# Optimization experiments

Hardware: AMD Instinct MI355X
Metric: run time of the kernel (lower is better)

The kernel has to match this reference:

```python
import jax, jax.numpy as jnp
import numpy as np

B, S, E, H, L = 4, 512, 768, 12, 12
D = E // H
FF = 4 * E
EPS = 1e-5
SCALE = jnp.float32(768.0 ** 0.5)  # emb_size ** (1/2), applied AFTER softmax per source


def setup_inputs() -> dict:
    key = jax.random.key(0)
    ks = jax.random.split(key, 18)
    std = 0.02
    n = lambda k, shp: (jax.random.normal(k, shp, jnp.float32) * std)
    return {
        "x": jax.random.normal(ks[0], (B, S, E), jnp.float32),
        "Wqkv": n(ks[1], (L, E, 3 * E)),
        "bqkv": n(ks[2], (L, 3 * E)),
        "Wp": n(ks[3], (L, E, E)),
        "bp": n(ks[4], (L, E)),
        "W1": n(ks[5], (L, E, FF)),
        "b1": n(ks[6], (L, FF)),
        "W2": n(ks[7], (L, FF, E)),
        "b2": n(ks[8], (L, E)),
        "ln1_g": jnp.ones((L, E), jnp.float32), "ln1_b": jnp.zeros((L, E), jnp.float32),
        "ln2_g": jnp.ones((L, E), jnp.float32), "ln2_b": jnp.zeros((L, E), jnp.float32),
        "ln3_g": jnp.ones((L, E), jnp.float32), "ln3_b": jnp.zeros((L, E), jnp.float32),
        "ln4_g": jnp.ones((L, E), jnp.float32), "ln4_b": jnp.zeros((L, E), jnp.float32),
    }


def _ln(x, g, b):
    m = jnp.mean(x, axis=-1, keepdims=True)
    v = jnp.mean(jnp.square(x - m), axis=-1, keepdims=True)
    return (x - m) * jax.lax.rsqrt(v + EPS) * g + b


def _block(x, p):
    Wqkv, bqkv, Wp, bp, W1, b1, W2, b2, g1, be1, g2, be2, g3, be3, g4, be4 = p
    # --- attention branch ---
    h = _ln(x, g1, be1)
    qkv = h @ Wqkv + bqkv                      # [B,S,3E]
    qkv = qkv.reshape(B, S, H, D, 3)           # qkv is innermost factor in source rearrange
    q = jnp.transpose(qkv[..., 0], (0, 2, 1, 3))  # [B,H,S,D]
    k = jnp.transpose(qkv[..., 1], (0, 2, 1, 3))
    v = jnp.transpose(qkv[..., 2], (0, 2, 1, 3))
    energy = jnp.einsum('bhqd,bhkd->bhqk', q, k)
    att = jax.nn.softmax(energy, axis=-1) / SCALE  # NOTE: scaling AFTER softmax (faithful)
    o = jnp.einsum('bhqk,bhkd->bhqd', att, v)
    o = jnp.transpose(o, (0, 2, 1, 3)).reshape(B, S, E)
    o = o @ Wp + bp
    r1 = _ln(o, g2, be2) + x                   # first ResidualAdd (final LN inside branch)
    # --- feed-forward branch ---
    f = _ln(r1, g3, be3)
    f = jax.nn.gelu(f @ W1 + b1, approximate=False)
    f = f @ W2 + b2
    r2 = _ln(f, g4, be4) + r1                  # second ResidualAdd
    return x + r2                              # outer residual: x = x + block(x)


def reference(x, Wqkv, bqkv, Wp, bp, W1, b1, W2, b2,
              ln1_g, ln1_b, ln2_g, ln2_b, ln3_g, ln3_b, ln4_g, ln4_b):
    params = (Wqkv, bqkv, Wp, bp, W1, b1, W2, b2,
              ln1_g, ln1_b, ln2_g, ln2_b, ln3_g, ln3_b, ln4_g, ln4_b)
    out, _ = jax.lax.scan(lambda c, p: (_block(c, p), None), x, params)
    return out
```

## Files before the change

### kernel.cpp

```cpp
#include <hip/hip_runtime.h>
#include <hip/hip_bf16.h>
#include <stdint.h>

#define LAYERS 12
#define M_ROWS 2048
#define E_DIM 768
#define FF_DIM 3072
#define QKV_DIM 2304
#define SCALE_INV 0.036084391824351615f

typedef __hip_bfloat16 bf16;
typedef __attribute__((ext_vector_type(8))) __bf16 bf16x8;
typedef __attribute__((ext_vector_type(4))) float f32x4;

__device__ __forceinline__ float bf2f(bf16 v) { return __bfloat162float(v); }
__device__ __forceinline__ bf16 f2bf(float v) { return __float2bfloat16(v); }

__device__ __forceinline__ float gelu_f(float x) {
  return 0.5f * x * (1.0f + erff(x * 0.70710678118654752f));
}

__device__ __forceinline__ void glds16(const bf16* g, bf16* l) {
  __builtin_amdgcn_global_load_lds(
      (const __attribute__((address_space(1))) void*)g,
      (__attribute__((address_space(3))) void*)l, 16, 0, 0);
}

__global__ __launch_bounds__(256) void transpose_k(
    const float* __restrict__ w0, const float* __restrict__ w1,
    const float* __restrict__ w2, const float* __restrict__ w3,
    bf16* __restrict__ t0, bf16* __restrict__ t1,
    bf16* __restrict__ t2, bf16* __restrict__ t3)
{
  __shared__ float T[32][33];
  int l = blockIdx.x / 6912;
  int bid = blockIdx.x - l * 6912;
  const float* src; bf16* dst; int K, N, tile;
  if (bid < 1728)      { src = w0 + (size_t)l * 768 * 2304; dst = t0 + (size_t)l * 768 * 2304; K = 768;  N = 2304; tile = bid; }
  else if (bid < 2304) { src = w1 + (size_t)l * 768 * 768;  dst = t1 + (size_t)l * 768 * 768;  K = 768;  N = 768;  tile = bid - 1728; }
  else if (bid < 4608) { src = w2 + (size_t)l * 768 * 3072; dst = t2 + (size_t)l * 768 * 3072; K = 768;  N = 3072; tile = bid - 2304; }
  else                 { src = w3 + (size_t)l * 3072 * 768; dst = t3 + (size_t)l * 3072 * 768; K = 3072; N = 768;  tile = bid - 4608; }
  int tilesN = N >> 5;
  int tk = tile / tilesN;
  int tn = tile - tk * tilesN;
  int tx = threadIdx.x & 31, ty = threadIdx.x >> 5;
  int k0 = tk << 5, n0 = tn << 5;
#pragma unroll
  for (int i = 0; i < 4; i++)
    T[ty + i * 8][tx] = src[(size_t)(k0 + ty + i * 8) * N + n0 + tx];
  __syncthreads();
#pragma unroll
  for (int i = 0; i < 4; i++)
    dst[(size_t)(n0 + ty + i * 8) * K + k0 + tx] = f2bf(T[tx][ty + i * 8]);
}

__device__ __forceinline__ void rowstats(float s, float sq, float* red, int tid,
                                         float& mean, float& rstd) {
#pragma unroll
  for (int off = 32; off; off >>= 1) {
    s += __shfl_xor(s, off);
    sq += __shfl_xor(sq, off);
  }
  __syncthreads();
  int wv = tid >> 6;
  if ((tid & 63) == 0) { red[wv] = s; red[4 + wv] = sq; }
  __syncthreads();
  s  = red[0] + red[1] + red[2] + red[3];
  sq = red[4] + red[5] + red[6] + red[7];
  mean = s * (1.0f / 768.0f);
  float var = sq * (1.0f / 768.0f) - mean * mean;
  rstd = rsqrtf(var + 1e-5f);
}

__global__ __launch_bounds__(256) void ln_k(
    const float* in, const float* gamma, const float* beta, bf16* outp)
{
  __shared__ float red[8];
  int row = blockIdx.x, tid = threadIdx.x;
  const float* x = in + (size_t)row * 768;
  float v[3]; float s = 0.f, sq = 0.f;
#pragma unroll
  for (int j = 0; j < 3; j++) {
    v[j] = x[tid + j * 256];
    s += v[j]; sq += v[j] * v[j];
  }
  float mean, rstd;
  rowstats(s, sq, red, tid, mean, rstd);
#pragma unroll
  for (int j = 0; j < 3; j++) {
    int c = tid + j * 256;
    outp[(size_t)row * 768 + c] = f2bf((v[j] - mean) * rstd * gamma[c] + beta[c]);
  }
}

__global__ __launch_bounds__(256) void ln23_k(
    const float* in, const float* g2, const float* b2, const float* xres,
    float* r1out, const float* g3, const float* b3, bf16* hbout)
{
  __shared__ float red[8];
  int row = blockIdx.x, tid = threadIdx.x;
  const float* x = in + (size_t)row * 768;
  float v[3]; float s = 0.f, sq = 0.f;
#pragma unroll
  for (int j = 0; j < 3; j++) {
    v[j] = x[tid + j * 256];
    s += v[j]; sq += v[j] * v[j];
  }
  float mean, rstd;
  rowstats(s, sq, red, tid, mean, rstd);
  s = 0.f; sq = 0.f;
#pragma unroll
  for (int j = 0; j < 3; j++) {
    int c = tid + j * 256;
    v[j] = (v[j] - mean) * rstd * g2[c] + b2[c] + xres[(size_t)row * 768 + c];
    r1out[(size_t)row * 768 + c] = v[j];
    s += v[j]; sq += v[j] * v[j];
  }
  rowstats(s, sq, red, tid, mean, rstd);
#pragma unroll
  for (int j = 0; j < 3; j++) {
    int c = tid + j * 256;
    hbout[(size_t)row * 768 + c] = f2bf((v[j] - mean) * rstd * g3[c] + b3[c]);
  }
}

__global__ __launch_bounds__(256) void ln41_k(
    const float* in, const float* g4, const float* b4, const float* r1,
    float* xio, const float* g1n, const float* b1n, bf16* hbout)
{
  __shared__ float red[8];
  int row = blockIdx.x, tid = threadIdx.x;
  const float* x = in + (size_t)row * 768;
  float v[3]; float s = 0.f, sq = 0.f;
#pragma unroll
  for (int j = 0; j < 3; j++) {
    v[j] = x[tid + j * 256];
    s += v[j]; sq += v[j] * v[j];
  }
  float mean, rstd;
  rowstats(s, sq, red, tid, mean, rstd);
  s = 0.f; sq = 0.f;
#pragma unroll
  for (int j = 0; j < 3; j++) {
    int c = tid + j * 256;
    size_t idx = (size_t)row * 768 + c;
    v[j] = (v[j] - mean) * rstd * g4[c] + b4[c] + r1[idx] + xio[idx];
    xio[idx] = v[j];
    s += v[j]; sq += v[j] * v[j];
  }
  if (g1n == nullptr) return;
  rowstats(s, sq, red, tid, mean, rstd);
#pragma unroll
  for (int j = 0; j < 3; j++) {
    int c = tid + j * 256;
    hbout[(size_t)row * 768 + c] = f2bf((v[j] - mean) * rstd * g1n[c] + b1n[c]);
  }
}

template<int OUT_MODE>
__global__ __launch_bounds__(256) void gemm128_k(
    const bf16* __restrict__ A, const bf16* __restrict__ BT,
    const float* __restrict__ bias, void* __restrict__ Cout,
    bf16* __restrict__ qo, bf16* __restrict__ ko, bf16* __restrict__ vo,
    int N, int K, int nTilesN)
{
  __shared__ __align__(16) bf16 Als[128 * 32];
  __shared__ __align__(16) bf16 Bls[128 * 32];
  int tid = threadIdx.x;
  int lane = tid & 63, w = tid >> 6;
  int l15 = lane & 15, l4 = lane >> 4;
  int tm = blockIdx.x / nTilesN;
  int tn = blockIdx.x - tm * nTilesN;
  int m0 = tm << 7, n0 = tn << 7;
  int wm = (w >> 1) << 6, wn = (w & 1) << 6;
  const bf16* Ag = A + (size_t)m0 * K;
  const bf16* Bg = BT + (size_t)n0 * K;
  int srow = tid >> 2;
  int scol = (tid & 3) * 8;
  f32x4 acc[4][4] = {};
  for (int k0 = 0; k0 < K; k0 += 32) {
    __syncthreads();
    glds16(Ag + (size_t)srow * K + k0 + scol,        Als + tid * 8);
    glds16(Ag + (size_t)(srow + 64) * K + k0 + scol, Als + 2048 + tid * 8);
    glds16(Bg + (size_t)srow * K + k0 + scol,        Bls + tid * 8);
    glds16(Bg + (size_t)(srow + 64) * K + k0 + scol, Bls + 2048 + tid * 8);
    __syncthreads();
    int ko8 = l4 * 8;
    bf16x8 af[4], bfr[4];
#pragma unroll
    for (int i = 0; i < 4; i++)
      af[i] = *(const bf16x8*)&Als[(wm + i * 16 + l15) * 32 + ko8];
#pragma unroll
    for (int j = 0; j < 4; j++)
      bfr[j] = *(const bf16x8*)&Bls[(wn + j * 16 + l15) * 32 + ko8];
#pragma unroll
    for (int i = 0; i < 4; i++)
#pragma unroll
      for (int j = 0; j < 4; j++)
        acc[i][j] = __builtin_amdgcn_mfma_f32_16x16x32_bf16(af[i], bfr[j], acc[i][j], 0, 0, 0);
  }
#pragma unroll
  for (int i = 0; i < 4; i++) {
    int mbase = m0 + wm + i * 16 + (l4 << 2);
#pragma unroll
    for (int j = 0; j < 4; j++) {
      int n = n0 + wn + j * 16 + l15;
      float bvs = bias[n];
      if (OUT_MODE == 3) {
        int h = n / 192;
        int rm = n - h * 192;
        int d = rm / 3;
        int t = rm - d * 3;
#pragma unroll
        for (int rg = 0; rg < 4; rg++) {
          int m = mbase + rg;
          float val = acc[i][j][rg] + bvs;
          int b = m >> 9, sIdx = m & 511;
          int bh = b * 12 + h;
          if (t == 2)
            vo[(size_t)((bh << 6) + d) * 512 + sIdx] = f2bf(val);
          else {
            bf16* dsts = (t == 0) ? qo : ko;
            dsts[(size_t)((bh << 9) + sIdx) * 64 + d] = f2bf(val);
          }
        }
      } else {
#pragma unroll
        for (int rg = 0; rg < 4; rg++) {
          int m = mbase + rg;
          float val = acc[i][j][rg] + bvs;
          ((bf16*)Cout)[(size_t)m * N + n] = f2bf(gelu_f(val));
        }
      }
    }
  }
}

__global__ __launch_bounds__(256) void gemm64_k(
    const bf16* __restrict__ A, const bf16* __restrict__ BT,
    const float* __restrict__ bias, float* __restrict__ Cout,
    int N, int K, int nTilesN)
{
  __shared__ __align__(16) bf16 Als[64 * 32];
  __shared__ __align__(16) bf16 Bls[64 * 32];
  int tid = threadIdx.x;
  int lane = tid & 63, w = tid >> 6;
  int l15 = lane & 15, l4 = lane >> 4;
  int tm = blockIdx.x / nTilesN;
  int tn = blockIdx.x - tm * nTilesN;
  int m0 = tm << 6, n0 = tn << 6;
  int wm = (w >> 1) << 5, wn = (w & 1) << 5;
  const bf16* Ag = A + (size_t)m0 * K;
  const bf16* Bg = BT + (size_t)n0 * K;
  int srow = tid >> 2;
  int scol = (tid & 3) * 8;
  f32x4 acc[2][2] = {};
  for (int k0 = 0; k0 < K; k0 += 32) {
    __syncthreads();
    glds16(Ag + (size_t)srow * K + k0 + scol, Als + tid * 8);
    glds16(Bg + (size_t)srow * K + k0 + scol, Bls + tid * 8);
    __syncthreads();
    int ko8 = l4 * 8;
    bf16x8 af[2], bfr[2];
#pragma unroll
    for (int i = 0; i < 2; i++)
      af[i] = *(const bf16x8*)&Als[(wm + i * 16 + l15) * 32 + ko8];
#pragma unroll
    for (int j = 0; j < 2; j++)
      bfr[j] = *(const bf16x8*)&Bls[(wn + j * 16 + l15) * 32 + ko8];
#pragma unroll
    for (int i = 0; i < 2; i++)
#pragma unroll
      for (int j = 0; j < 2; j++)
        acc[i][j] = __builtin_amdgcn_mfma_f32_16x16x32_bf16(af[i], bfr[j], acc[i][j], 0, 0, 0);
  }
#pragma unroll
  for (int i = 0; i < 2; i++) {
    int mbase = m0 + wm + i * 16 + (l4 << 2);
#pragma unroll
    for (int j = 0; j < 2; j++) {
      int n = n0 + wn + j * 16 + l15;
      float bvs = bias[n];
#pragma unroll
      for (int rg = 0; rg < 4; rg++)
        Cout[(size_t)(mbase + rg) * N + n] = acc[i][j][rg] + bvs;
    }
  }
}

#define PSTR 80
__global__ __launch_bounds__(256) void attn_k(
    const bf16* __restrict__ q, const bf16* __restrict__ k,
    const bf16* __restrict__ vT, bf16* __restrict__ o)
{
  __shared__ __align__(16) bf16 Kls[64 * 64];
  __shared__ __align__(16) bf16 Vls[64 * 64];
  __shared__ __align__(16) bf16 Pls[4][16 * PSTR];
  int tid = threadIdx.x;
  int lane = tid & 63, w = tid >> 6;
  int l15 = lane & 15, l4 = lane >> 4;
  int qt = blockIdx.x & 7;
  int bh = blockIdx.x >> 3;
  size_t base = (size_t)bh * 32768;

  const bf16* qrowp = q + base + (size_t)(qt * 64 + w * 16 + l15) * 64 + l4 * 8;
  bf16x8 qf0 = *(const bf16x8*)qrowp;
  bf16x8 qf1 = *(const bf16x8*)(qrowp + 32);

  float mrow[4] = {-1e30f, -1e30f, -1e30f, -1e30f};
  float lsum[4] = {0.f, 0.f, 0.f, 0.f};
  f32x4 Oacc[4] = {};
  const f32x4 zed = {0.f, 0.f, 0.f, 0.f};
  bf16* pw = &Pls[w][0];

  for (int kt = 0; kt < 8; kt++) {
    __syncthreads();
#pragma unroll
    for (int rep = 0; rep < 2; rep++) {
      int c = tid + rep * 256;
      int row = c >> 3, col8 = (c & 7) * 8;
      *(uint4*)&Kls[row * 64 + col8] =
          *(const uint4*)(k + base + (size_t)(kt * 64 + row) * 64 + col8);
      *(uint4*)&Vls[row * 64 + col8] =
          *(const uint4*)(vT + base + (size_t)row * 512 + kt * 64 + col8);
    }
    __syncthreads();
    f32x4 e[4];
#pragma unroll
    for (int jt = 0; jt < 4; jt++) {
      bf16x8 kf0 = *(const bf16x8*)&Kls[(jt * 16 + l15) * 64 + l4 * 8];
      bf16x8 kf1 = *(const bf16x8*)&Kls[(jt * 16 + l15) * 64 + l4 * 8 + 32];
      e[jt] = __builtin_amdgcn_mfma_f32_16x16x32_bf16(qf0, kf0, zed, 0, 0, 0);
      e[jt] = __builtin_amdgcn_mfma_f32_16x16x32_bf16(qf1, kf1, e[jt], 0, 0, 0);
    }
    float al[4];
#pragma unroll
    for (int rg = 0; rg < 4; rg++) {
      float mn = fmaxf(fmaxf(e[0][rg], e[1][rg]), fmaxf(e[2][rg], e[3][rg]));
#pragma unroll
      for (int off = 1; off < 16; off <<= 1) mn = fmaxf(mn, __shfl_xor(mn, off));
      float mnew = fmaxf(mrow[rg], mn);
      al[rg] = __expf(mrow[rg] - mnew);
      mrow[rg] = mnew;
    }
    float rs[4] = {0.f, 0.f, 0.f, 0.f};
#pragma unroll
    for (int jt = 0; jt < 4; jt++)
#pragma unroll
      for (int rg = 0; rg < 4; rg++) {
        float p = __expf(e[jt][rg] - mrow[rg]);
        rs[rg] += p;
        pw[(l4 * 4 + rg) * PSTR + jt * 16 + l15] = f2bf(p);
      }
#pragma unroll
    for (int rg = 0; rg < 4; rg++) {
#pragma unroll
      for (int off = 1; off < 16; off <<= 1) rs[rg] += __shfl_xor(rs[rg], off);
      lsum[rg] = lsum[rg] * al[rg] + rs[rg];
    }
#pragma unroll
    for (int dt = 0; dt < 4; dt++)
#pragma unroll
      for (int rg = 0; rg < 4; rg++) Oacc[dt][rg] *= al[rg];
    bf16x8 pf0 = *(const bf16x8*)&pw[l15 * PSTR + l4 * 8];
    bf16x8 pf1 = *(const bf16x8*)&pw[l15 * PSTR + l4 * 8 + 32];
#pragma unroll
    for (int dt = 0; dt < 4; dt++) {
      bf16x8 vf0 = *(const bf16x8*)&Vls[(dt * 16 + l15) * 64 + l4 * 8];
      bf16x8 vf1 = *(const bf16x8*)&Vls[(dt * 16 + l15) * 64 + l4 * 8 + 32];
      Oacc[dt] = __builtin_amdgcn_mfma_f32_16x16x32_bf16(pf0, vf0, Oacc[dt], 0, 0, 0);
      Oacc[dt] = __builtin_amdgcn_mfma_f32_16x16x32_bf16(pf1, vf1, Oacc[dt], 0, 0, 0);
    }
  }
  int b = bh / 12, h = bh - b * 12;
#pragma unroll
  for (int rg = 0; rg < 4; rg++) {
    int qrow = qt * 64 + w * 16 + l4 * 4 + rg;
    float inv = SCALE_INV / lsum[rg];
    size_t rowoff = (size_t)(b * 512 + qrow) * 768 + h * 64;
#pragma unroll
    for (int dt = 0; dt < 4; dt++)
      o[rowoff + dt * 16 + l15] = f2bf(Oacc[dt][rg] * inv);
  }
}

extern "C" void kernel_launch(void* const* d_in, const int* in_sizes, int n_in,
                              void* d_out, int out_size, void* d_ws, size_t ws_size,
                              hipStream_t stream)
{
  const float* x    = (const float*)d_in[0];
  const float* Wqkv = (const float*)d_in[1];
  const float* bqkv = (const float*)d_in[2];
  const float* Wp   = (const float*)d_in[3];
  const float* bp   = (const float*)d_in[4];
  const float* W1   = (const float*)d_in[5];
  const float* b1   = (const float*)d_in[6];
  const float* W2   = (const float*)d_in[7];
  const float* b2   = (const float*)d_in[8];
  const float* g1  = (const float*)d_in[9];
  const float* be1 = (const float*)d_in[10];
  const float* g2  = (const float*)d_in[11];
  const float* be2 = (const float*)d_in[12];
  const float* g3  = (const float*)d_in[13];
  const float* be3 = (const float*)d_in[14];
  const float* g4  = (const float*)d_in[15];
  const float* be4 = (const float*)d_in[16];
  float* xout = (float*)d_out;

  char* ws = (char*)d_ws;
  size_t off = 0;
  auto alloc = [&](size_t bytes) -> char* {
    char* p = ws + off;
    off += (bytes + 255) & ~(size_t)255;
    return p;
  };
  const size_t NTOK = (size_t)M_ROWS * E_DIM;
  bf16*  qb  = (bf16*)alloc(NTOK * 2);
  bf16*  kb  = (bf16*)alloc(NTOK * 2);
  bf16*  vb  = (bf16*)alloc(NTOK * 2);
  bf16*  hb  = (bf16*)alloc(NTOK * 2);
  bf16*  ob  = (bf16*)alloc(NTOK * 2);
  bf16*  f1b = (bf16*)alloc((size_t)M_ROWS * FF_DIM * 2);
  float* tmp = (float*)alloc(NTOK * 4);
  float* r1  = (float*)alloc(NTOK * 4);
  bf16*  tq  = (bf16*)alloc((size_t)LAYERS * 768 * 2304 * 2);
  bf16*  tp  = (bf16*)alloc((size_t)LAYERS * 768 * 768 * 2);
  bf16*  t1  = (bf16*)alloc((size_t)LAYERS * 768 * 3072 * 2);
  bf16*  t2  = (bf16*)alloc((size_t)LAYERS * 3072 * 768 * 2);
  if (off > ws_size) {
    hipMemsetAsync(d_out, 0x7f, (size_t)out_size * 4, stream);
    return;
  }

  hipMemcpyAsync(d_out, x, (size_t)out_size * 4, hipMemcpyDeviceToDevice, stream);

  transpose_k<<<6912 * LAYERS, 256, 0, stream>>>(Wqkv, Wp, W1, W2, tq, tp, t1, t2);

  ln_k<<<2048, 256, 0, stream>>>(xout, g1, be1, hb);

  for (int l = 0; l < LAYERS; l++) {
    const bf16* tql = tq + (size_t)l * 768 * 2304;
    const bf16* tpl = tp + (size_t)l * 768 * 768;
    const bf16* t1l = t1 + (size_t)l * 768 * 3072;
    const bf16* t2l = t2 + (size_t)l * 3072 * 768;

    gemm128_k<3><<<16 * 18, 256, 0, stream>>>(hb, tql, bqkv + (size_t)l * QKV_DIM,
                                              nullptr, qb, kb, vb, QKV_DIM, 768, 18);
    attn_k<<<384, 256, 0, stream>>>(qb, kb, vb, ob);
    gemm64_k<<<32 * 12, 256, 0, stream>>>(ob, tpl, bp + (size_t)l * 768,
                                          tmp, 768, 768, 12);
    ln23_k<<<2048, 256, 0, stream>>>(tmp, g2 + l * 768, be2 + l * 768, xout,
                                     r1, g3 + l * 768, be3 + l * 768, hb);
    gemm128_k<2><<<16 * 24, 256, 0, stream>>>(hb, t1l, b1 + (size_t)l * FF_DIM,
                                              f1b, nullptr, nullptr, nullptr, FF_DIM, 768, 24);
    gemm64_k<<<32 * 12, 256, 0, stream>>>(f1b, t2l, b2 + (size_t)l * 768,
                                          tmp, 768, 3072, 12);
    const float* g1n  = (l + 1 < LAYERS) ? g1 + (l + 1) * 768 : nullptr;
    const float* be1n = (l + 1 < LAYERS) ? be1 + (l + 1) * 768 : nullptr;
    ln41_k<<<2048, 256, 0, stream>>>(tmp, g4 + l * 768, be4 + l * 768, r1,
                                     xout, g1n, be1n, hb);
  }
}
```

Measured before the change: 2.320 ms.

## Shrink GEMM N-tile to 64, stage through registers, vectorize weight transpose

Three separate changes. The QKV and FF1 GEMMs move from 128x128 to 128x64 tiles, doubling the block count so more of the CUs get work. Both GEMM kernels now load global tiles into registers before the barrier and then write them to LDS, replacing the direct global-to-LDS loads; this lets the global load latency overlap the previous iteration's barrier. The weight transpose uses 64x64 tiles with float4 reads and 16-byte bf16 writes to cut block count and memory transactions, at the cost of higher register pressure and lower per-block MFMA reuse.

New measurement: 2.232 ms. -3.8%, faster.

```diff
diff --git a/kernel.cpp b/kernel.cpp
--- a/kernel.cpp
+++ b/kernel.cpp
@@ -20,38 +20,47 @@
   return 0.5f * x * (1.0f + erff(x * 0.70710678118654752f));
 }
 
-__device__ __forceinline__ void glds16(const bf16* g, bf16* l) {
-  __builtin_amdgcn_global_load_lds(
-      (const __attribute__((address_space(1))) void*)g,
-      (__attribute__((address_space(3))) void*)l, 16, 0, 0);
-}
-
 __global__ __launch_bounds__(256) void transpose_k(
     const float* __restrict__ w0, const float* __restrict__ w1,
     const float* __restrict__ w2, const float* __restrict__ w3,
     bf16* __restrict__ t0, bf16* __restrict__ t1,
     bf16* __restrict__ t2, bf16* __restrict__ t3)
 {
-  __shared__ float T[32][33];
-  int l = blockIdx.x / 6912;
-  int bid = blockIdx.x - l * 6912;
+  __shared__ float T[64][68];
+  int l = blockIdx.x / 1728;
+  int bid = blockIdx.x - l * 1728;
   const float* src; bf16* dst; int K, N, tile;
-  if (bid < 1728)      { src = w0 + (size_t)l * 768 * 2304; dst = t0 + (size_t)l * 768 * 2304; K = 768;  N = 2304; tile = bid; }
-  else if (bid < 2304) { src = w1 + (size_t)l * 768 * 768;  dst = t1 + (size_t)l * 768 * 768;  K = 768;  N = 768;  tile = bid - 1728; }
-  else if (bid < 4608) { src = w2 + (size_t)l * 768 * 3072; dst = t2 + (size_t)l * 768 * 3072; K = 768;  N = 3072; tile = bid - 2304; }
-  else                 { src = w3 + (size_t)l * 3072 * 768; dst = t3 + (size_t)l * 3072 * 768; K = 3072; N = 768;  tile = bid - 4608; }
-  int tilesN = N >> 5;
+  if (bid < 432)      { src = w0 + (size_t)l * 768 * 2304; dst = t0 + (size_t)l * 768 * 2304; K = 768;  N = 2304; tile = bid; }
+  else if (bid < 576) { src = w1 + (size_t)l * 768 * 768;  dst = t1 + (size_t)l * 768 * 768;  K = 768;  N = 768;  tile = bid - 432; }
+  else if (bid < 1152){ src = w2 + (size_t)l * 768 * 3072; dst = t2 + (size_t)l * 768 * 3072; K = 768;  N = 3072; tile = bid - 576; }
+  else                { src = w3 + (size_t)l * 3072 * 768; dst = t3 + (size_t)l * 3072 * 768; K = 3072; N = 768;  tile = bid - 1152; }
+  int tilesN = N >> 6;
   int tk = tile / tilesN;
   int tn = tile - tk * tilesN;
-  int tx = threadIdx.x & 31, ty = threadIdx.x >> 5;
-  int k0 = tk << 5, n0 = tn << 5;
-#pragma unroll
-  for (int i = 0; i < 4; i++)
-    T[ty + i * 8][tx] = src[(size_t)(k0 + ty + i * 8) * N + n0 + tx];
+  int k0 = tk << 6, n0 = tn << 6;
+  int tid = threadIdx.x;
+  int tr = tid >> 2;
+  int tc = (tid & 3) * 16;
+#pragma unroll
+  for (int i = 0; i < 4; i++) {
+    float4 f4 = *(const float4*)&src[(size_t)(k0 + tr) * N + n0 + tc + i * 4];
+    T[tc + i * 4 + 0][tr] = f4.x;
+    T[tc + i * 4 + 1][tr] = f4.y;
+    T[tc + i * 4 + 2][tr] = f4.z;
+    T[tc + i * 4 + 3][tr] = f4.w;
+  }
   __syncthreads();
-#pragma unroll
-  for (int i = 0; i < 4; i++)
-    dst[(size_t)(n0 + ty + i * 8) * K + k0 + tx] = f2bf(T[tx][ty + i * 8]);
+  bf16 outv[16];
+#pragma unroll
+  for (int i = 0; i < 4; i++) {
+    float4 f4 = *(const float4*)&T[tr][tc + i * 4];
+    outv[i * 4 + 0] = f2bf(f4.x);
+    outv[i * 4 + 1] = f2bf(f4.y);
+    outv[i * 4 + 2] = f2bf(f4.z);
+    outv[i * 4 + 3] = f2bf(f4.w);
+  }
+  *(uint4*)&dst[(size_t)(n0 + tr) * K + k0 + tc] = *(uint4*)&outv[0];
+  *(uint4*)&dst[(size_t)(n0 + tr) * K + k0 + tc + 8] = *(uint4*)&outv[8];
 }
 
 __device__ __forceinline__ void rowstats(float s, float sq, float* red, int tid,
@@ -158,53 +167,55 @@
 }
 
 template<int OUT_MODE>
-__global__ __launch_bounds__(256) void gemm128_k(
+__global__ __launch_bounds__(256) void gemm_mn_k(
     const bf16* __restrict__ A, const bf16* __restrict__ BT,
     const float* __restrict__ bias, void* __restrict__ Cout,
     bf16* __restrict__ qo, bf16* __restrict__ ko, bf16* __restrict__ vo,
     int N, int K, int nTilesN)
 {
   __shared__ __align__(16) bf16 Als[128 * 32];
-  __shared__ __align__(16) bf16 Bls[128 * 32];
+  __shared__ __align__(16) bf16 Bls[64 * 32];
   int tid = threadIdx.x;
   int lane = tid & 63, w = tid >> 6;
   int l15 = lane & 15, l4 = lane >> 4;
   int tm = blockIdx.x / nTilesN;
   int tn = blockIdx.x - tm * nTilesN;
-  int m0 = tm << 7, n0 = tn << 7;
-  int wm = (w >> 1) << 6, wn = (w & 1) << 6;
+  int m0 = tm << 7, n0 = tn << 6;
+  int wm = w << 5;
   const bf16* Ag = A + (size_t)m0 * K;
   const bf16* Bg = BT + (size_t)n0 * K;
   int srow = tid >> 2;
   int scol = (tid & 3) * 8;
-  f32x4 acc[4][4] = {};
+  f32x4 acc[2][4] = {};
   for (int k0 = 0; k0 < K; k0 += 32) {
-    __syncthreads();
-    glds16(Ag + (size_t)srow * K + k0 + scol,        Als + tid * 8);
-    glds16(Ag + (size_t)(srow + 64) * K + k0 + scol, Als + 2048 + tid * 8);
-    glds16(Bg + (size_t)srow * K + k0 + scol,        Bls + tid * 8);
-    glds16(Bg + (size_t)(srow + 64) * K + k0 + scol, Bls + 2048 + tid * 8);
+    uint4 av0 = *(const uint4*)(Ag + (size_t)srow * K + k0 + scol);
+    uint4 av1 = *(const uint4*)(Ag + (size_t)(srow + 64) * K + k0 + scol);
+    uint4 bv  = *(const uint4*)(Bg + (size_t)srow * K + k0 + scol);
+    __syncthreads();
+    *(uint4*)&Als[tid * 8] = av0;
+    *(uint4*)&Als[2048 + tid * 8] = av1;
+    *(uint4*)&Bls[tid * 8] = bv;
     __syncthreads();
     int ko8 = l4 * 8;
-    bf16x8 af[4], bfr[4];
-#pragma unroll
-    for (int i = 0; i < 4; i++)
+    bf16x8 af[2], bfr[4];
+#pragma unroll
+    for (int i = 0; i < 2; i++)
       af[i] = *(const bf16x8*)&Als[(wm + i * 16 + l15) * 32 + ko8];
 #pragma unroll
     for (int j = 0; j < 4; j++)
-      bfr[j] = *(const bf16x8*)&Bls[(wn + j * 16 + l15) * 32 + ko8];
-#pragma unroll
-    for (int i = 0; i < 4; i++)
+      bfr[j] = *(const bf16x8*)&Bls[(j * 16 + l15) * 32 + ko8];
+#pragma unroll
+    for (int i = 0; i < 2; i++)
 #pragma unroll
       for (int j = 0; j < 4; j++)
         acc[i][j] = __builtin_amdgcn_mfma_f32_16x16x32_bf16(af[i], bfr[j], acc[i][j], 0, 0, 0);
   }
 #pragma unroll
-  for (int i = 0; i < 4; i++) {
+  for (int i = 0; i < 2; i++) {
     int mbase = m0 + wm + i * 16 + (l4 << 2);
 #pragma unroll
     for (int j = 0; j < 4; j++) {
-      int n = n0 + wn + j * 16 + l15;
+      int n = n0 + j * 16 + l15;
       float bvs = bias[n];
       if (OUT_MODE == 3) {
         int h = n / 192;
@@ -256,9 +267,11 @@
   int scol = (tid & 3) * 8;
   f32x4 acc[2][2] = {};
   for (int k0 = 0; k0 < K; k0 += 32) {
-    __syncthreads();
-    glds16(Ag + (size_t)srow * K + k0 + scol, Als + tid * 8);
-    glds16(Bg + (size_t)srow * K + k0 + scol, Bls + tid * 8);
+    uint4 av = *(const uint4*)(Ag + (size_t)srow * K + k0 + scol);
+    uint4 bv = *(const uint4*)(Bg + (size_t)srow * K + k0 + scol);
+    __syncthreads();
+    *(uint4*)&Als[tid * 8] = av;
+    *(uint4*)&Bls[tid * 8] = bv;
     __syncthreads();
     int ko8 = l4 * 8;
     bf16x8 af[2], bfr[2];
@@ -434,8 +447,7 @@
 
   hipMemcpyAsync(d_out, x, (size_t)out_size * 4, hipMemcpyDeviceToDevice, stream);
 
-  transpose_k<<<6912 * LAYERS, 256, 0, stream>>>(Wqkv, Wp, W1, W2, tq, tp, t1, t2);
-
+  transpose_k<<<1728 * LAYERS, 256, 0, stream>>>(Wqkv, Wp, W1, W2, tq, tp, t1, t2);
   ln_k<<<2048, 256, 0, stream>>>(xout, g1, be1, hb);
 
   for (int l = 0; l < LAYERS; l++) {
@@ -444,15 +456,15 @@
     const bf16* t1l = t1 + (size_t)l * 768 * 3072;
     const bf16* t2l = t2 + (size_t)l * 3072 * 768;
 
-    gemm128_k<3><<<16 * 18, 256, 0, stream>>>(hb, tql, bqkv + (size_t)l * QKV_DIM,
-                                              nullptr, qb, kb, vb, QKV_DIM, 768, 18);
+    gemm_mn_k<3><<<16 * 36, 256, 0, stream>>>(hb, tql, bqkv + (size_t)l * QKV_DIM,
+                                              nullptr, qb, kb, vb, QKV_DIM, 768, 36);
     attn_k<<<384, 256, 0, stream>>>(qb, kb, vb, ob);
     gemm64_k<<<32 * 12, 256, 0, stream>>>(ob, tpl, bp + (size_t)l * 768,
                                           tmp, 768, 768, 12);
     ln23_k<<<2048, 256, 0, stream>>>(tmp, g2 + l * 768, be2 + l * 768, xout,
                                      r1, g3 + l * 768, be3 + l * 768, hb);
-    gemm128_k<2><<<16 * 24, 256, 0, stream>>>(hb, t1l, b1 + (size_t)l * FF_DIM,
-                                              f1b, nullptr, nullptr, nullptr, FF_DIM, 768, 24);
+    gemm_mn_k<2><<<16 * 48, 256, 0, stream>>>(hb, t1l, b1 + (size_t)l * FF_DIM,
+                                              f1b, nullptr, nullptr, nullptr, FF_DIM, 768, 48);
     gemm64_k<<<32 * 12, 256, 0, stream>>>(f1b, t2l, b2 + (size_t)l * 768,
                                           tmp, 768, 3072, 12);
     const float* g1n  = (l + 1 < LAYERS) ? g1 + (l + 1) * 768 : nullptr;
```
